# Performance work log

Hardware: AMD Instinct MI355X
Metric: run time of the kernel (lower is better)

## Reference

```python
import jax, jax.numpy as jnp
import numpy as np

D_MODEL = 1024
NUM_HEADS = 16
D_K = D_MODEL // NUM_HEADS
B, S = 4, 2048


def setup_inputs() -> dict:
    key = jax.random.key(0)
    ks = jax.random.split(key, 11)
    scale = 1.0 / np.sqrt(D_MODEL)
    inp = {
        "query": jax.random.normal(ks[0], (B, S, D_MODEL), dtype=jnp.float32),
        "key": jax.random.normal(ks[1], (B, S, D_MODEL), dtype=jnp.float32),
        "value": jax.random.normal(ks[2], (B, S, D_MODEL), dtype=jnp.float32),
        "mask": jnp.ones((B, 1, S, S), dtype=bool),
        "W_q": jax.random.normal(ks[3], (D_MODEL, D_MODEL), dtype=jnp.float32) * scale,
        "b_q": jax.random.normal(ks[4], (D_MODEL,), dtype=jnp.float32) * 0.01,
        "W_k": jax.random.normal(ks[5], (D_MODEL, D_MODEL), dtype=jnp.float32) * scale,
        "b_k": jax.random.normal(ks[6], (D_MODEL,), dtype=jnp.float32) * 0.01,
        "W_v": jax.random.normal(ks[7], (D_MODEL, D_MODEL), dtype=jnp.float32) * scale,
        "b_v": jax.random.normal(ks[8], (D_MODEL,), dtype=jnp.float32) * 0.01,
        "W_o": jax.random.normal(ks[9], (D_MODEL, D_MODEL), dtype=jnp.float32) * scale,
        "b_o": jax.random.normal(ks[10], (D_MODEL,), dtype=jnp.float32) * 0.01,
    }
    return inp


def _split_heads(x):
    # [B, S, d_model] -> [B, H, S, d_k]
    b, s, _ = x.shape
    return x.reshape(b, s, NUM_HEADS, D_K).transpose(0, 2, 1, 3)


def reference(query, key, value, mask, W_q, b_q, W_k, b_k, W_v, b_v, W_o, b_o):
    q = _split_heads(query @ W_q.T + b_q)
    k = _split_heads(key @ W_k.T + b_k)
    v = _split_heads(value @ W_v.T + b_v)
    # scores: [B, H, S, S]
    scores = jnp.einsum("bhqd,bhkd->bhqk", q, k) / jnp.sqrt(jnp.float32(D_K))
    scores = jnp.where(mask, scores, jnp.float32(-1e9))
    attn = jax.nn.softmax(scores, axis=-1)
    out = jnp.einsum("bhqk,bhkd->bhqd", attn, v)  # [B, H, S, d_k]
    out = out.transpose(0, 2, 1, 3).reshape(query.shape[0], -1, NUM_HEADS * D_K)
    return out @ W_o.T + b_o
```

## Files before the change

kernel.cpp:

```cpp
#include <hip/hip_runtime.h>
#include <hip/hip_bf16.h>

#define SEQ 2048
#define NHEADS 16
#define DK 64
#define DMODEL 1024
#define MTOK 8192
#define WN (DMODEL * DMODEL)

typedef __attribute__((ext_vector_type(4))) float f32x4;
typedef __attribute__((ext_vector_type(8))) short shortx8;
typedef __attribute__((ext_vector_type(4))) short shortx4;
typedef __attribute__((ext_vector_type(8))) unsigned short ushortx8;

typedef __attribute__((address_space(3))) unsigned int lds_uint;
typedef const __attribute__((address_space(1))) unsigned int glob_uint;

__device__ __forceinline__ unsigned pack_bf2(float a, float b) {
  union { __hip_bfloat162 h; unsigned u; } c;
  c.h = __float22bfloat162_rn(float2{a, b});
  return c.u;
}

__device__ __forceinline__ unsigned short f2bf(float f) {
  union { __hip_bfloat16 h; unsigned short u; } c;
  c.h = __float2bfloat16(f);
  return c.u;
}

__device__ __forceinline__ ushortx8 cvt8(float4 f0, float4 f1) {
  union { ushortx8 v; unsigned u[4]; } c;
  c.u[0] = pack_bf2(f0.x, f0.y);
  c.u[1] = pack_bf2(f0.z, f0.w);
  c.u[2] = pack_bf2(f1.x, f1.y);
  c.u[3] = pack_bf2(f1.z, f1.w);
  return c.v;
}

__device__ __forceinline__ float exp2a(float x) {
  float r;
  asm("v_exp_f32 %0, %1" : "=v"(r) : "v"(x));
  return r;
}

__device__ __forceinline__ float fmax3f(float a, float b, float c) {
  return fmaxf(fmaxf(a, b), c);
}

__device__ __forceinline__ int vperm64(int s6) {
  return (s6 & 35) | ((s6 & 12) << 1) | ((s6 & 16) >> 2);
}

struct ConvSeg { const float* src; unsigned short* dst; int n8; };
struct ConvArgs { ConvSeg s[7]; };

__global__ __launch_bounds__(256) void convert_bf16(ConvArgs a, int nseg) {
  const int y = blockIdx.y;
  if (y >= nseg) return;
  const ConvSeg seg = a.s[y];
  const int stride = gridDim.x * blockDim.x;
  for (int i = blockIdx.x * blockDim.x + threadIdx.x; i < seg.n8; i += stride) {
    const float4 f0 = ((const float4*)seg.src)[(size_t)i * 2];
    const float4 f1 = ((const float4*)seg.src)[(size_t)i * 2 + 1];
    ((ushortx8*)seg.dst)[i] = cvt8(f0, f1);
  }
}

template<int OUT_MODE>
__global__ __launch_bounds__(256) void gemm_lds(
    const unsigned short* __restrict__ A,
    const unsigned short* __restrict__ Bw,
    const float* __restrict__ bias, void* __restrict__ outp,
    int M, int N, int K)
{
  constexpr int BM = 128, BN = 128, BK = 32;
  __shared__ __align__(16) unsigned short As[2][BM][BK];
  __shared__ __align__(16) unsigned short Bs[2][BN][BK];

  const int tid = threadIdx.x, wave = tid >> 6, lane = tid & 63;
  const int nblk = N / BN;
  const int cpx = gridDim.x >> 3;
  const int id = (blockIdx.x & 7) * cpx + (blockIdx.x >> 3);
  const int n0 = (id % nblk) * BN, m0 = (id / nblk) * BM;
  const int wr0 = (wave >> 1) * 64, wc0 = (wave & 1) * 64;
  const int lrow = lane & 15, kk8 = (lane >> 4) * 8;
  const int sr = lane >> 2, sc = (lane & 3) * 8;

  const unsigned short* Ag = A  + (size_t)(m0 + wave * 32 + sr) * K + sc;
  const unsigned short* Bg = Bw + (size_t)(n0 + wave * 32 + sr) * K + sc;

  auto stage = [&](int buf) {
    __builtin_amdgcn_global_load_lds((glob_uint*)Ag,
        (lds_uint*)&As[buf][wave * 32][0], 16, 0, 0);
    __builtin_amdgcn_global_load_lds((glob_uint*)(Ag + (size_t)16 * K),
        (lds_uint*)&As[buf][wave * 32 + 16][0], 16, 0, 0);
    __builtin_amdgcn_global_load_lds((glob_uint*)Bg,
        (lds_uint*)&Bs[buf][wave * 32][0], 16, 0, 0);
    __builtin_amdgcn_global_load_lds((glob_uint*)(Bg + (size_t)16 * K),
        (lds_uint*)&Bs[buf][wave * 32 + 16][0], 16, 0, 0);
    Ag += BK; Bg += BK;
  };

  f32x4 acc[4][4] = {};
  const int nt = K / BK;

  stage(0);
  stage(1);

  for (int t = 0; t < nt; ++t) {
    const int cur = t & 1;
    if (t < nt - 1) asm volatile("s_waitcnt vmcnt(4)" ::: "memory");
    else            asm volatile("s_waitcnt vmcnt(0)" ::: "memory");
    __builtin_amdgcn_s_barrier();

    shortx8 af[4], bf[4];
    #pragma unroll
    for (int i = 0; i < 4; ++i) {
      af[i] = *(const shortx8*)&As[cur][wr0 + i*16 + lrow][kk8];
      bf[i] = *(const shortx8*)&Bs[cur][wc0 + i*16 + lrow][kk8];
    }
    asm volatile("s_waitcnt lgkmcnt(0)" ::: "memory");
    __builtin_amdgcn_sched_barrier(0);
    __builtin_amdgcn_s_barrier();

    if (t + 2 < nt) stage(cur);

    __builtin_amdgcn_s_setprio(1);
    #pragma unroll
    for (int mi = 0; mi < 4; ++mi)
      #pragma unroll
      for (int ni = 0; ni < 4; ++ni)
        acc[mi][ni] = __builtin_amdgcn_mfma_f32_16x16x32_bf16(af[mi], bf[ni], acc[mi][ni], 0, 0, 0);
    __builtin_amdgcn_s_setprio(0);
  }

  #pragma unroll
  for (int mi = 0; mi < 4; ++mi) {
    #pragma unroll
    for (int ni = 0; ni < 4; ++ni) {
      #pragma unroll
      for (int r = 0; r < 4; ++r) {
        const int row = m0 + wr0 + mi*16 + (lane >> 4) * 4 + r;
        const int col = n0 + wc0 + ni*16 + lrow;
        const float v = acc[mi][ni][r] + bias[col];
        if constexpr (OUT_MODE == 1) {
          const int b = row >> 11, s = row & 2047, h = col >> 6, d = col & 63;
          ((unsigned short*)outp)[(((size_t)(b * NHEADS + h)) * SEQ + s) * DK + d] = f2bf(v);
        } else if constexpr (OUT_MODE == 2) {
          const int b = row >> 11, s = row & 2047, h = col >> 6, d = col & 63;
          const int sp = (s & ~63) | vperm64(s & 63);
          ((unsigned short*)outp)[(((size_t)(b * NHEADS + h)) * DK + d) * SEQ + sp] = f2bf(v);
        } else {
          ((float*)outp)[(size_t)row * N + col] = v;
        }
      }
    }
  }
}

template<int OUT_MODE, bool A_BF16>
__global__ __launch_bounds__(256) void gemm_bt(
    const void* __restrict__ Xv, const float* __restrict__ W,
    const float* __restrict__ bias, void* __restrict__ outp,
    int M, int N, int K)
{
  constexpr int BM = 128, BN = 128, BK = 32;
  constexpr int LD = BK + 8;
  __shared__ __align__(16) unsigned short As[BM][LD];
  __shared__ __align__(16) unsigned short Bs[BN][LD];

  const int tid  = threadIdx.x;
  const int wave = tid >> 6, lane = tid & 63;
  const int m0 = blockIdx.x * BM, n0 = blockIdx.y * BN;
  const int wr0 = (wave >> 1) * 64, wc0 = (wave & 1) * 64;
  const int lrow = lane & 15, kk8 = (lane >> 4) * 8;

  f32x4 acc[4][4] = {};
  const int srow = tid >> 2;
  const int scol = (tid & 3) * 8;

  for (int k0 = 0; k0 < K; k0 += BK) {
    #pragma unroll
    for (int it = 0; it < 2; ++it) {
      const int row = srow + it * 64;
      ushortx8 pa;
      if constexpr (A_BF16) {
        pa = *(const ushortx8*)((const unsigned short*)Xv + (size_t)(m0 + row) * K + k0 + scol);
      } else {
        const float* s = (const float*)Xv + (size_t)(m0 + row) * K + k0 + scol;
        pa = cvt8(*(const float4*)s, *(const float4*)(s + 4));
      }
      *(ushortx8*)&As[row][scol] = pa;
      const float* ws_ = W + (size_t)(n0 + row) * K + k0 + scol;
      *(ushortx8*)&Bs[row][scol] = cvt8(*(const float4*)ws_, *(const float4*)(ws_ + 4));
    }
    __syncthreads();

    shortx8 af[4], bf[4];
    #pragma unroll
    for (int i = 0; i < 4; ++i) {
      af[i] = *(const shortx8*)&As[wr0 + i*16 + lrow][kk8];
      bf[i] = *(const shortx8*)&Bs[wc0 + i*16 + lrow][kk8];
    }
    #pragma unroll
    for (int mi = 0; mi < 4; ++mi)
      #pragma unroll
      for (int ni = 0; ni < 4; ++ni)
        acc[mi][ni] = __builtin_amdgcn_mfma_f32_16x16x32_bf16(af[mi], bf[ni], acc[mi][ni], 0, 0, 0);
    __syncthreads();
  }

  #pragma unroll
  for (int mi = 0; mi < 4; ++mi) {
    #pragma unroll
    for (int ni = 0; ni < 4; ++ni) {
      #pragma unroll
      for (int r = 0; r < 4; ++r) {
        const int row = m0 + wr0 + mi*16 + (lane >> 4) * 4 + r;
        const int col = n0 + wc0 + ni*16 + lrow;
        const float v = acc[mi][ni][r] + bias[col];
        if constexpr (OUT_MODE == 0) {
          ((unsigned short*)outp)[(size_t)row * N + col] = f2bf(v);
        } else if constexpr (OUT_MODE == 1) {
          const int b = row >> 11, s = row & 2047, h = col >> 6, d = col & 63;
          ((unsigned short*)outp)[(((size_t)(b * NHEADS + h)) * SEQ + s) * DK + d] = f2bf(v);
        } else if constexpr (OUT_MODE == 2) {
          const int b = row >> 11, s = row & 2047, h = col >> 6, d = col & 63;
          const int sp = (s & ~63) | vperm64(s & 63);
          ((unsigned short*)outp)[(((size_t)(b * NHEADS + h)) * DK + d) * SEQ + sp] = f2bf(v);
        } else {
          ((float*)outp)[(size_t)row * N + col] = v;
        }
      }
    }
  }
}

__global__ __launch_bounds__(256, 4) void flash_attn(
    const unsigned short* __restrict__ Q,
    const unsigned short* __restrict__ Kg,
    const unsigned short* __restrict__ Vt,
    unsigned short* __restrict__ O)
{
  constexpr int KVB = 64;
  constexpr int LD = 64 + 8;
  constexpr int NT = SEQ / KVB;
  constexpr float C2 = 0.18033688011112042f;
  __shared__ __align__(16) unsigned short Ks[2][KVB][LD];
  __shared__ __align__(16) unsigned short Vs[2][DK][LD];

  const int tid = threadIdx.x, wave = tid >> 6, lane = tid & 63;
  const int id = blockIdx.x;
  const int bh = (id & 7) * 8 + (id >> 7);
  const int qx = (id >> 3) & 15;
  const int b = bh >> 4, h = bh & 15;
  const int q0 = qx * 128;
  const int lrow = lane & 15, g = lane >> 4, kk8 = g * 8;

  const unsigned short* Qb = Q  + (size_t)bh * SEQ * DK;
  const unsigned short* Kb = Kg + (size_t)bh * SEQ * DK;
  const unsigned short* Vb = Vt + (size_t)bh * DK * SEQ;

  shortx8 qf[2][2];
  #pragma unroll
  for (int qt = 0; qt < 2; ++qt) {
    const unsigned short* qs = Qb + (size_t)(q0 + wave * 32 + qt * 16 + lrow) * DK + kk8;
    qf[qt][0] = *(const shortx8*)qs;
    qf[qt][1] = *(const shortx8*)(qs + 32);
  }

  shortx8 vones;
  #pragma unroll
  for (int j = 0; j < 8; ++j) vones[j] = (short)0x3F80;

  f32x4 oacc[2][4] = {};
  f32x4 oextra[2] = {};
  float mrun[2] = {-3e38f, -3e38f};

  const int srow = tid >> 2;
  const int scol = (tid & 3) * 16;

  const unsigned short* kptr = Kb + (size_t)srow * DK + scol;
  const unsigned short* vptr = Vb + (size_t)srow * SEQ + scol;
  {
    *(ushortx8*)&Ks[0][srow][scol]     = *(const ushortx8*)kptr;
    *(ushortx8*)&Ks[0][srow][scol + 8] = *(const ushortx8*)(kptr + 8);
    *(ushortx8*)&Vs[0][srow][scol]     = *(const ushortx8*)vptr;
    *(ushortx8*)&Vs[0][srow][scol + 8] = *(const ushortx8*)(vptr + 8);
  }
  kptr += KVB * DK; vptr += KVB;
  __syncthreads();

  for (int t = 0; t < NT; ++t) {
    const int cur = t & 1;
    const bool pre = (t + 1 < NT);

    ushortx8 sk0, sk1, sv0, sv1;
    if (pre) {
      sk0 = *(const ushortx8*)kptr;
      sk1 = *(const ushortx8*)(kptr + 8);
      sv0 = *(const ushortx8*)vptr;
      sv1 = *(const ushortx8*)(vptr + 8);
      kptr += KVB * DK; vptr += KVB;
    }

    f32x4 sacc[2][4] = {};
    __builtin_amdgcn_s_setprio(1);
    #pragma unroll
    for (int nt = 0; nt < 4; ++nt) {
      shortx8 kf0 = *(const shortx8*)&Ks[cur][nt*16 + lrow][kk8];
      shortx8 kf1 = *(const shortx8*)&Ks[cur][nt*16 + lrow][32 + kk8];
      #pragma unroll
      for (int qt = 0; qt < 2; ++qt) {
        sacc[qt][nt] = __builtin_amdgcn_mfma_f32_16x16x32_bf16(kf0, qf[qt][0], sacc[qt][nt], 0, 0, 0);
        sacc[qt][nt] = __builtin_amdgcn_mfma_f32_16x16x32_bf16(kf1, qf[qt][1], sacc[qt][nt], 0, 0, 0);
      }
    }
    __builtin_amdgcn_s_setprio(0);

    shortx8 pfrag[2][2];
    #pragma unroll
    for (int qt = 0; qt < 2; ++qt) {
      const f32x4* s = sacc[qt];
      const float t0 = fmax3f(s[0][0], s[0][1], s[0][2]);
      const float t1 = fmax3f(s[0][3], s[1][0], s[1][1]);
      const float t2 = fmax3f(s[1][2], s[1][3], s[2][0]);
      const float t3 = fmax3f(s[2][1], s[2][2], s[2][3]);
      const float t4 = fmax3f(s[3][0], s[3][1], s[3][2]);
      const float t5 = fmax3f(t3, t4, s[3][3]);
      const float lm = fmaxf(fmax3f(t0, t1, t2), t5);

      if (__any(lm - mrun[qt] > 56.f)) {
        float pw = lm;
        pw = fmaxf(pw, __shfl_xor(pw, 16));
        pw = fmaxf(pw, __shfl_xor(pw, 32));
        const float m = fmaxf(mrun[qt], pw);
        const float fsc = exp2a((mrun[qt] - m) * C2);
        mrun[qt] = m;
        #pragma unroll
        for (int r = 0; r < 4; ++r) oextra[qt][r] *= fsc;
        #pragma unroll
        for (int dt = 0; dt < 4; ++dt)
          #pragma unroll
          for (int r = 0; r < 4; ++r)
            oacc[qt][dt][r] *= fsc;
      }
      const float mb = -mrun[qt] * C2;

      float p[4][4];
      #pragma unroll
      for (int nt = 0; nt < 4; ++nt)
        #pragma unroll
        for (int r = 0; r < 4; ++r)
          p[nt][r] = exp2a(__builtin_fmaf(sacc[qt][nt][r], C2, mb));

      #pragma unroll
      for (int ksp = 0; ksp < 2; ++ksp) {
        union { shortx8 sv; unsigned u[4]; } pf;
        pf.u[0] = pack_bf2(p[ksp*2][0],   p[ksp*2][1]);
        pf.u[1] = pack_bf2(p[ksp*2][2],   p[ksp*2][3]);
        pf.u[2] = pack_bf2(p[ksp*2+1][0], p[ksp*2+1][1]);
        pf.u[3] = pack_bf2(p[ksp*2+1][2], p[ksp*2+1][3]);
        pfrag[qt][ksp] = pf.sv;
      }
    }

    __builtin_amdgcn_s_setprio(1);
    #pragma unroll
    for (int dt = 0; dt < 4; ++dt) {
      #pragma unroll
      for (int ksp = 0; ksp < 2; ++ksp) {
        shortx8 bv = *(const shortx8*)&Vs[cur][dt*16 + lrow][ksp*32 + g*8];
        #pragma unroll
        for (int qt = 0; qt < 2; ++qt)
          oacc[qt][dt] = __builtin_amdgcn_mfma_f32_16x16x32_bf16(bv, pfrag[qt][ksp], oacc[qt][dt], 0, 0, 0);
      }
    }
    #pragma unroll
    for (int ksp = 0; ksp < 2; ++ksp)
      #pragma unroll
      for (int qt = 0; qt < 2; ++qt)
        oextra[qt] = __builtin_amdgcn_mfma_f32_16x16x32_bf16(vones, pfrag[qt][ksp], oextra[qt], 0, 0, 0);
    __builtin_amdgcn_s_setprio(0);

    if (pre) {
      const int nb = cur ^ 1;
      *(ushortx8*)&Ks[nb][srow][scol]     = sk0;
      *(ushortx8*)&Ks[nb][srow][scol + 8] = sk1;
      *(ushortx8*)&Vs[nb][srow][scol]     = sv0;
      *(ushortx8*)&Vs[nb][srow][scol + 8] = sv1;
    }
    __syncthreads();
  }

  #pragma unroll
  for (int qt = 0; qt < 2; ++qt) {
    const float inv = 1.f / oextra[qt][0];
    const int qrow = q0 + wave * 32 + qt * 16 + lrow;
    unsigned short* Orow = O + ((size_t)b * SEQ + qrow) * DMODEL + h * DK;
    #pragma unroll
    for (int dt = 0; dt < 4; ++dt) {
      uint2 w2;
      w2.x = pack_bf2(oacc[qt][dt][0] * inv, oacc[qt][dt][1] * inv);
      w2.y = pack_bf2(oacc[qt][dt][2] * inv, oacc[qt][dt][3] * inv);
      *(uint2*)&Orow[dt*16 + g*4] = w2;
    }
  }
}

extern "C" void kernel_launch(void* const* d_in, const int* in_sizes, int n_in,
                              void* d_out, int out_size, void* d_ws, size_t ws_size,
                              hipStream_t stream) {
  const float* query = (const float*)d_in[0];
  const float* key   = (const float*)d_in[1];
  const float* value = (const float*)d_in[2];
  const float* W_q = (const float*)d_in[4];
  const float* b_q = (const float*)d_in[5];
  const float* W_k = (const float*)d_in[6];
  const float* b_k = (const float*)d_in[7];
  const float* W_v = (const float*)d_in[8];
  const float* b_v = (const float*)d_in[9];
  const float* W_o = (const float*)d_in[10];
  const float* b_o = (const float*)d_in[11];

  const size_t XN = (size_t)MTOK * DMODEL;
  const size_t NEED1 = (4 * (size_t)WN + 6 * XN) * sizeof(unsigned short);
  const size_t NEED2 = (4 * (size_t)WN + 4 * XN) * sizeof(unsigned short);

  dim3 blk(256);

  if (ws_size >= NEED1) {
    unsigned short* wb    = (unsigned short*)d_ws;
    unsigned short* xq    = wb + 4 * (size_t)WN;
    unsigned short* xk    = xq + XN;
    unsigned short* xv    = xk + XN;
    unsigned short* q_ws  = xv + XN;
    unsigned short* k_ws  = q_ws + XN;
    unsigned short* vt_ws = k_ws + XN;
    unsigned short* a_ws  = xq;

    ConvArgs ca;
    ca.s[0] = {query, xq,        (int)(XN / 8)};
    ca.s[1] = {key,   xk,        (int)(XN / 8)};
    ca.s[2] = {value, xv,        (int)(XN / 8)};
    ca.s[3] = {W_q,   wb,        WN / 8};
    ca.s[4] = {W_k,   wb + WN,   WN / 8};
    ca.s[5] = {W_v,   wb + 2*WN, WN / 8};
    ca.s[6] = {W_o,   wb + 3*WN, WN / 8};
    convert_bf16<<<dim3(1024, 7), blk, 0, stream>>>(ca, 7);

    gemm_lds<1><<<dim3(512), blk, 0, stream>>>(xq, wb,        b_q, q_ws,  MTOK, DMODEL, DMODEL);
    gemm_lds<1><<<dim3(512), blk, 0, stream>>>(xk, wb + WN,   b_k, k_ws,  MTOK, DMODEL, DMODEL);
    gemm_lds<2><<<dim3(512), blk, 0, stream>>>(xv, wb + 2*WN, b_v, vt_ws, MTOK, DMODEL, DMODEL);

    flash_attn<<<dim3(1024), blk, 0, stream>>>(q_ws, k_ws, vt_ws, a_ws);

    gemm_lds<3><<<dim3(512), blk, 0, stream>>>(a_ws, wb + 3*WN, b_o, d_out,
                                               MTOK, DMODEL, DMODEL);
  } else if (ws_size >= NEED2) {
    unsigned short* xb    = (unsigned short*)d_ws;
    unsigned short* wb    = xb + XN;
    unsigned short* q_ws  = wb + 4 * (size_t)WN;
    unsigned short* k_ws  = q_ws + XN;
    unsigned short* vt_ws = k_ws + XN;
    unsigned short* a_ws  = xb;

    ConvArgs a1;
    a1.s[0] = {query, xb,        (int)(XN / 8)};
    a1.s[1] = {W_q,   wb,        WN / 8};
    a1.s[2] = {W_k,   wb + WN,   WN / 8};
    a1.s[3] = {W_v,   wb + 2*WN, WN / 8};
    a1.s[4] = {W_o,   wb + 3*WN, WN / 8};
    convert_bf16<<<dim3(1024, 5), blk, 0, stream>>>(a1, 5);
    gemm_lds<1><<<dim3(512), blk, 0, stream>>>(xb, wb, b_q, q_ws, MTOK, DMODEL, DMODEL);

    ConvArgs a2; a2.s[0] = {key, xb, (int)(XN / 8)};
    convert_bf16<<<dim3(2048, 1), blk, 0, stream>>>(a2, 1);
    gemm_lds<1><<<dim3(512), blk, 0, stream>>>(xb, wb + WN, b_k, k_ws, MTOK, DMODEL, DMODEL);

    ConvArgs a3; a3.s[0] = {value, xb, (int)(XN / 8)};
    convert_bf16<<<dim3(2048, 1), blk, 0, stream>>>(a3, 1);
    gemm_lds<2><<<dim3(512), blk, 0, stream>>>(xb, wb + 2*WN, b_v, vt_ws, MTOK, DMODEL, DMODEL);

    flash_attn<<<dim3(1024), blk, 0, stream>>>(q_ws, k_ws, vt_ws, a_ws);

    gemm_lds<3><<<dim3(512), blk, 0, stream>>>(a_ws, wb + 3*WN, b_o, d_out,
                                               MTOK, DMODEL, DMODEL);
  } else {
    unsigned short* q_ws  = (unsigned short*)d_ws;
    unsigned short* k_ws  = q_ws  + XN;
    unsigned short* vt_ws = k_ws  + XN;
    unsigned short* a_ws  = vt_ws + XN;

    dim3 gridg(MTOK / 128, DMODEL / 128);
    gemm_bt<1, false><<<gridg, blk, 0, stream>>>(query, W_q, b_q, q_ws,  MTOK, DMODEL, DMODEL);
    gemm_bt<1, false><<<gridg, blk, 0, stream>>>(key,   W_k, b_k, k_ws,  MTOK, DMODEL, DMODEL);
    gemm_bt<2, false><<<gridg, blk, 0, stream>>>(value, W_v, b_v, vt_ws, MTOK, DMODEL, DMODEL);
    flash_attn<<<dim3(1024), blk, 0, stream>>>(q_ws, k_ws, vt_ws, a_ws);
    gemm_bt<3, true><<<gridg, blk, 0, stream>>>(a_ws, W_o, b_o, d_out, MTOK, DMODEL, DMODEL);
  }
}
```

Baseline: 210.5 us.

## Stage K/V tiles via direct global-to-LDS loads with XOR-swizzled layout

The flash attention kernel now copies K and V tiles straight from global memory into LDS using global_load_lds, instead of going through registers and then storing to LDS. LDS padding is removed. To avoid bank conflicts without padding, the K and V projection GEMMs write their outputs pre-swizzled with an XOR pattern, and the attention kernel reads fragments with matching swizzled offsets. This saves register pressure and the extra LDS store instructions, but the pipeline now waits on vmcnt(0) and a barrier every iteration, which can expose load latency.

```diff
diff --git a/kernel.cpp b/kernel.cpp
--- a/kernel.cpp
+++ b/kernel.cpp
@@ -10,7 +10,6 @@
 
 typedef __attribute__((ext_vector_type(4))) float f32x4;
 typedef __attribute__((ext_vector_type(8))) short shortx8;
-typedef __attribute__((ext_vector_type(4))) short shortx4;
 typedef __attribute__((ext_vector_type(8))) unsigned short ushortx8;
 
 typedef __attribute__((address_space(3))) unsigned int lds_uint;
@@ -146,9 +145,14 @@
         if constexpr (OUT_MODE == 1) {
           const int b = row >> 11, s = row & 2047, h = col >> 6, d = col & 63;
           ((unsigned short*)outp)[(((size_t)(b * NHEADS + h)) * SEQ + s) * DK + d] = f2bf(v);
+        } else if constexpr (OUT_MODE == 4) {
+          const int b = row >> 11, s = row & 2047, h = col >> 6, d = col & 63;
+          const int d2 = d ^ ((s & 7) << 3);
+          ((unsigned short*)outp)[(((size_t)(b * NHEADS + h)) * SEQ + s) * DK + d2] = f2bf(v);
         } else if constexpr (OUT_MODE == 2) {
           const int b = row >> 11, s = row & 2047, h = col >> 6, d = col & 63;
-          const int sp = (s & ~63) | vperm64(s & 63);
+          int sp = (s & ~63) | vperm64(s & 63);
+          sp ^= (d & 7) << 3;
           ((unsigned short*)outp)[(((size_t)(b * NHEADS + h)) * DK + d) * SEQ + sp] = f2bf(v);
         } else {
           ((float*)outp)[(size_t)row * N + col] = v;
@@ -224,9 +228,14 @@
         } else if constexpr (OUT_MODE == 1) {
           const int b = row >> 11, s = row & 2047, h = col >> 6, d = col & 63;
           ((unsigned short*)outp)[(((size_t)(b * NHEADS + h)) * SEQ + s) * DK + d] = f2bf(v);
+        } else if constexpr (OUT_MODE == 4) {
+          const int b = row >> 11, s = row & 2047, h = col >> 6, d = col & 63;
+          const int d2 = d ^ ((s & 7) << 3);
+          ((unsigned short*)outp)[(((size_t)(b * NHEADS + h)) * SEQ + s) * DK + d2] = f2bf(v);
         } else if constexpr (OUT_MODE == 2) {
           const int b = row >> 11, s = row & 2047, h = col >> 6, d = col & 63;
-          const int sp = (s & ~63) | vperm64(s & 63);
+          int sp = (s & ~63) | vperm64(s & 63);
+          sp ^= (d & 7) << 3;
           ((unsigned short*)outp)[(((size_t)(b * NHEADS + h)) * DK + d) * SEQ + sp] = f2bf(v);
         } else {
           ((float*)outp)[(size_t)row * N + col] = v;
@@ -243,11 +252,10 @@
     unsigned short* __restrict__ O)
 {
   constexpr int KVB = 64;
-  constexpr int LD = 64 + 8;
   constexpr int NT = SEQ / KVB;
   constexpr float C2 = 0.18033688011112042f;
-  __shared__ __align__(16) unsigned short Ks[2][KVB][LD];
-  __shared__ __align__(16) unsigned short Vs[2][DK][LD];
+  __shared__ __align__(16) unsigned short Ks[2][KVB][64];
+  __shared__ __align__(16) unsigned short Vs[2][DK][64];
 
   const int tid = threadIdx.x, wave = tid >> 6, lane = tid & 63;
   const int id = blockIdx.x;
@@ -256,6 +264,8 @@
   const int b = bh >> 4, h = bh & 15;
   const int q0 = qx * 128;
   const int lrow = lane & 15, g = lane >> 4, kk8 = g * 8;
+  const int gA = ((g ^ (lrow & 7)) & 7) * 8;
+  const int gB = (((g ^ (lrow & 7)) ^ 4) & 7) * 8;
 
   const unsigned short* Qb = Q  + (size_t)bh * SEQ * DK;
   const unsigned short* Kb = Kg + (size_t)bh * SEQ * DK;
@@ -277,39 +287,37 @@
   f32x4 oextra[2] = {};
   float mrun[2] = {-3e38f, -3e38f};
 
-  const int srow = tid >> 2;
-  const int scol = (tid & 3) * 16;
-
-  const unsigned short* kptr = Kb + (size_t)srow * DK + scol;
-  const unsigned short* vptr = Vb + (size_t)srow * SEQ + scol;
-  {
-    *(ushortx8*)&Ks[0][srow][scol]     = *(const ushortx8*)kptr;
-    *(ushortx8*)&Ks[0][srow][scol + 8] = *(const ushortx8*)(kptr + 8);
-    *(ushortx8*)&Vs[0][srow][scol]     = *(const ushortx8*)vptr;
-    *(ushortx8*)&Vs[0][srow][scol + 8] = *(const ushortx8*)(vptr + 8);
-  }
-  kptr += KVB * DK; vptr += KVB;
-  __syncthreads();
+  const int srow16 = wave * 16 + (lane >> 3);
+  const int sg8 = (lane & 7) * 8;
+  const unsigned short* ksrc = Kb + (size_t)srow16 * DK + sg8;
+  const unsigned short* vsrc = Vb + (size_t)srow16 * SEQ + sg8;
+
+  auto stage = [&](int buf) {
+    __builtin_amdgcn_global_load_lds((glob_uint*)ksrc,
+        (lds_uint*)&Ks[buf][wave * 16][0], 16, 0, 0);
+    __builtin_amdgcn_global_load_lds((glob_uint*)(ksrc + (size_t)8 * DK),
+        (lds_uint*)&Ks[buf][wave * 16 + 8][0], 16, 0, 0);
+    __builtin_amdgcn_global_load_lds((glob_uint*)vsrc,
+        (lds_uint*)&Vs[buf][wave * 16][0], 16, 0, 0);
+    __builtin_amdgcn_global_load_lds((glob_uint*)(vsrc + (size_t)8 * SEQ),
+        (lds_uint*)&Vs[buf][wave * 16 + 8][0], 16, 0, 0);
+    ksrc += KVB * DK; vsrc += KVB;
+  };
+
+  stage(0);
+  stage(1);
+  asm volatile("s_waitcnt vmcnt(0)" ::: "memory");
+  __builtin_amdgcn_s_barrier();
 
   for (int t = 0; t < NT; ++t) {
     const int cur = t & 1;
-    const bool pre = (t + 1 < NT);
-
-    ushortx8 sk0, sk1, sv0, sv1;
-    if (pre) {
-      sk0 = *(const ushortx8*)kptr;
-      sk1 = *(const ushortx8*)(kptr + 8);
-      sv0 = *(const ushortx8*)vptr;
-      sv1 = *(const ushortx8*)(vptr + 8);
-      kptr += KVB * DK; vptr += KVB;
-    }
 
     f32x4 sacc[2][4] = {};
     __builtin_amdgcn_s_setprio(1);
     #pragma unroll
     for (int nt = 0; nt < 4; ++nt) {
-      shortx8 kf0 = *(const shortx8*)&Ks[cur][nt*16 + lrow][kk8];
-      shortx8 kf1 = *(const shortx8*)&Ks[cur][nt*16 + lrow][32 + kk8];
+      shortx8 kf0 = *(const shortx8*)&Ks[cur][nt*16 + lrow][gA];
+      shortx8 kf1 = *(const shortx8*)&Ks[cur][nt*16 + lrow][gB];
       #pragma unroll
       for (int qt = 0; qt < 2; ++qt) {
         sacc[qt][nt] = __builtin_amdgcn_mfma_f32_16x16x32_bf16(kf0, qf[qt][0], sacc[qt][nt], 0, 0, 0);
@@ -370,7 +378,7 @@
     for (int dt = 0; dt < 4; ++dt) {
       #pragma unroll
       for (int ksp = 0; ksp < 2; ++ksp) {
-        shortx8 bv = *(const shortx8*)&Vs[cur][dt*16 + lrow][ksp*32 + g*8];
+        shortx8 bv = *(const shortx8*)&Vs[cur][dt*16 + lrow][ksp ? gB : gA];
         #pragma unroll
         for (int qt = 0; qt < 2; ++qt)
           oacc[qt][dt] = __builtin_amdgcn_mfma_f32_16x16x32_bf16(bv, pfrag[qt][ksp], oacc[qt][dt], 0, 0, 0);
@@ -383,14 +391,9 @@
         oextra[qt] = __builtin_amdgcn_mfma_f32_16x16x32_bf16(vones, pfrag[qt][ksp], oextra[qt], 0, 0, 0);
     __builtin_amdgcn_s_setprio(0);
 
-    if (pre) {
-      const int nb = cur ^ 1;
-      *(ushortx8*)&Ks[nb][srow][scol]     = sk0;
-      *(ushortx8*)&Ks[nb][srow][scol + 8] = sk1;
-      *(ushortx8*)&Vs[nb][srow][scol]     = sv0;
-      *(ushortx8*)&Vs[nb][srow][scol + 8] = sv1;
-    }
-    __syncthreads();
+    asm volatile("s_waitcnt vmcnt(0)" ::: "memory");
+    __builtin_amdgcn_s_barrier();
+    if (t + 2 < NT) stage(cur);
   }
 
   #pragma unroll
@@ -450,7 +453,7 @@
     convert_bf16<<<dim3(1024, 7), blk, 0, stream>>>(ca, 7);
 
     gemm_lds<1><<<dim3(512), blk, 0, stream>>>(xq, wb,        b_q, q_ws,  MTOK, DMODEL, DMODEL);
-    gemm_lds<1><<<dim3(512), blk, 0, stream>>>(xk, wb + WN,   b_k, k_ws,  MTOK, DMODEL, DMODEL);
+    gemm_lds<4><<<dim3(512), blk, 0, stream>>>(xk, wb + WN,   b_k, k_ws,  MTOK, DMODEL, DMODEL);
     gemm_lds<2><<<dim3(512), blk, 0, stream>>>(xv, wb + 2*WN, b_v, vt_ws, MTOK, DMODEL, DMODEL);
 
     flash_attn<<<dim3(1024), blk, 0, stream>>>(q_ws, k_ws, vt_ws, a_ws);
@@ -476,7 +479,7 @@
 
     ConvArgs a2; a2.s[0] = {key, xb, (int)(XN / 8)};
     convert_bf16<<<dim3(2048, 1), blk, 0, stream>>>(a2, 1);
-    gemm_lds<1><<<dim3(512), blk, 0, stream>>>(xb, wb + WN, b_k, k_ws, MTOK, DMODEL, DMODEL);
+    gemm_lds<4><<<dim3(512), blk, 0, stream>>>(xb, wb + WN, b_k, k_ws, MTOK, DMODEL, DMODEL);
 
     ConvArgs a3; a3.s[0] = {value, xb, (int)(XN / 8)};
     convert_bf16<<<dim3(2048, 1), blk, 0, stream>>>(a3, 1);
@@ -494,7 +497,7 @@
 
     dim3 gridg(MTOK / 128, DMODEL / 128);
     gemm_bt<1, false><<<gridg, blk, 0, stream>>>(query, W_q, b_q, q_ws,  MTOK, DMODEL, DMODEL);
-    gemm_bt<1, false><<<gridg, blk, 0, stream>>>(key,   W_k, b_k, k_ws,  MTOK, DMODEL, DMODEL);
+    gemm_bt<4, false><<<gridg, blk, 0, stream>>>(key,   W_k, b_k, k_ws,  MTOK, DMODEL, DMODEL);
     gemm_bt<2, false><<<gridg, blk, 0, stream>>>(value, W_v, b_v, vt_ws, MTOK, DMODEL, DMODEL);
     flash_attn<<<dim3(1024), blk, 0, stream>>>(q_ws, k_ws, vt_ws, a_ws);
     gemm_bt<3, true><<<gridg, blk, 0, stream>>>(a_ws, W_o, b_o, d_out, MTOK, DMODEL, DMODEL);
```

Result: slower. 220.3 us (+4.6%).
